# Performance work log

Measured on AMD Instinct MI355X. Metric: run time of the kernel, lower is better.

The kernel has to match this reference:

```python
import jax, jax.numpy as jnp
import numpy as np

PAD = 24
DR0, DR1 = 425.0, 905.0
DDIM = 128.0
N = 65536
H, W, D, FDIM = 176, 176, 132, 32
LAT, OUT, INP = 128, 257, 3
NUM_LAYERS = 8
SKIP = 4


def _linear_params(k, out_f, in_f):
    kw, kb = jax.random.split(k)
    s = 1.0 / np.sqrt(in_f)
    Wm = jax.random.uniform(kw, (out_f, in_f), jnp.float32, -s, s)
    bv = jax.random.uniform(kb, (out_f,), jnp.float32, -s, s)
    return Wm, bv


def setup_inputs() -> dict:
    key = jax.random.key(0)
    ks = jax.random.split(key, 20)
    world = jax.random.normal(ks[0], (N, 3), jnp.float32)
    u = jax.random.uniform(ks[1], (N,), jnp.float32, 2.0, 125.0)
    v = jax.random.uniform(ks[2], (N,), jnp.float32, 2.0, 125.0)
    d = jax.random.uniform(ks[3], (N,), jnp.float32, 440.0, 890.0)
    pixel = jnp.stack([u, v, d], axis=1)
    vol = jax.random.uniform(ks[4], (H, W, D, FDIM), jnp.float32)
    Wq, bq = _linear_params(ks[5], LAT, FDIM)
    inp = dict(sampled_points_world=world, sampled_points_pixel=pixel,
               feature_volume=vol, Wq=Wq, bq=bq)
    # MLP: layer0 3->128; layers 1..8: layer 4 is 128->125, else 128->128; layer9 128->257
    dims = [(LAT, INP)]
    for i in range(NUM_LAYERS):
        dims.append((LAT - INP if (i + 1) == SKIP else LAT, LAT))
    dims.append((OUT, LAT))
    for l, (o, i) in enumerate(dims):
        Wl, bl = _linear_params(ks[6 + l], o, i)
        inp[f"W{l}"] = Wl
        inp[f"b{l}"] = bl
    return inp


def softplus100(x):
    # torch Softplus(beta=100) with threshold=20: linear when 100*x > 20
    return jnp.where(x > 0.2, x, jnp.log1p(jnp.exp(jnp.minimum(x, 0.2) * 100.0)) / 100.0)


def query_layer(pixel, vol, Wq, bq):
    # q: padded/depth-normalized query coords [N,3]
    q = jnp.stack([pixel[:, 0] + PAD, pixel[:, 1] + PAD,
                   (pixel[:, 2] - DR0) / (DR1 - DR0) * DDIM], axis=1)
    base = jnp.floor(q).astype(jnp.int32)            # center = floor+0.5 for non-integer coords
    ax = jnp.arange(-1, 3)                           # window floor-1 .. floor+2 (4 per axis)
    offs = jnp.stack(jnp.meshgrid(ax, ax, ax, indexing='ij'), -1).reshape(-1, 3)  # [64,3]
    idx = base[:, None, :] + offs[None, :, :]        # [N,64,3]
    kcoord = idx.astype(q.dtype)
    vfeat = vol[idx[..., 0], idx[..., 1], idx[..., 2]]   # [N,64,F] gather
    sim = jnp.einsum('nkd,nd->nk', kcoord, q)            # key . query
    sim = sim / jnp.sum(sim, axis=1, keepdims=True)
    mixed = jnp.einsum('nk,nkf->nf', sim, vfeat)         # [N,F]
    feat = mixed / jnp.sum(mixed, axis=1, keepdims=True)
    return feat @ Wq.T + bq                              # [N,128]


def reference(sampled_points_world, sampled_points_pixel, feature_volume, Wq, bq,
              W0, b0, W1, b1, W2, b2, W3, b3, W4, b4,
              W5, b5, W6, b6, W7, b7, W8, b8, W9, b9):
    Ws = [W0, W1, W2, W3, W4, W5, W6, W7, W8, W9]
    bs = [b0, b1, b2, b3, b4, b5, b6, b7, b8, b9]
    bias = query_layer(sampled_points_pixel, feature_volume, Wq, bq)
    bias = bias / jnp.mean(jnp.abs(bias))
    x = sampled_points_world
    for l in range(NUM_LAYERS + 2):
        x = x @ Ws[l].T + bs[l]
        if l == SKIP:
            x = jnp.concatenate([x, sampled_points_world], axis=1)
        if l == 0:
            x = x * bias
        if l < NUM_LAYERS + 1:
            x = softplus100(x)
    return x
```

## Files before the change

kernel.cpp:

```cpp
#include <hip/hip_runtime.h>

#define NPTS 65536
#define VW 176
#define VD 132
#define FD 32

typedef _Float16 half8 __attribute__((ext_vector_type(8)));
typedef _Float16 h16x4 __attribute__((ext_vector_type(4)));
typedef float f32x4 __attribute__((ext_vector_type(4)));

#define OFF_WQ 0
#define OFF_L1 4096
#define OFF_L9 (4096 + 8 * 16384)
#define W16_TOTAL (4096 + 8 * 16384 + 32768)

struct Params {
    const float* W[10];
    const float* b[10];
};

__device__ __forceinline__ float sp100(float x) {
    if (x > 0.2f) return x;
    float e = __expf(x * 100.0f);
    return __logf(1.0f + e) * 0.01f;
}

__global__ __launch_bounds__(256) void prep_kernel(Params P, const float* __restrict__ Wq,
                                                   _Float16* __restrict__ w16) {
    const int i = blockIdx.x * 256 + threadIdx.x;
    if (i >= W16_TOTAL) return;
    if (i < 4096) { w16[i] = (_Float16)Wq[i]; return; }
    int j = i - 4096;
    if (j < 8 * 16384) {
        const int l = (j >> 14) + 1;
        const int r = (j & 16383) >> 7;
        float v = 0.0f;
        if (l != 4) v = P.W[l][j & 16383];
        else if (r < 125) v = P.W[4][j & 16383];
        w16[i] = (_Float16)v;
        return;
    }
    j -= 8 * 16384;
    w16[i] = (_Float16)P.W[9][j];
}

__global__ __launch_bounds__(256) void query_kernel(
    const float* __restrict__ pixel, const float* __restrict__ vol,
    _Float16* __restrict__ feat_out)
{
    const int tid = threadIdx.x;
    const int f = tid & 31;
    const int p = blockIdx.x * 8 + (tid >> 5);

    const float qx = pixel[p*3+0] + 24.0f;
    const float qy = pixel[p*3+1] + 24.0f;
    const float qz = (pixel[p*3+2] - 425.0f) / 480.0f * 128.0f;
    const int bx = (int)floorf(qx);
    const int by = (int)floorf(qy);
    const int bz = (int)floorf(qz);

    float mix0 = 0.0f, mix1 = 0.0f;
    #pragma unroll
    for (int dx = 0; dx < 4; ++dx) {
        const int i0 = bx + dx - 1;
        const float sx = (float)i0 * qx;
        #pragma unroll
        for (int dy = 0; dy < 4; ++dy) {
            const int i1 = by + dy - 1;
            const int rowbase = (i0 * VW + i1) * VD;
            const float sxy = sx + (float)i1 * qy;
            #pragma unroll
            for (int dz = 0; dz < 4; ++dz) {
                const int i2 = bz + dz - 1;
                const float sim = sxy + (float)i2 * qz;
                const float v = vol[(rowbase + i2) * FD + f];
                if (dx < 2) mix0 = fmaf(sim, v, mix0);
                else        mix1 = fmaf(sim, v, mix1);
            }
        }
    }
    const float mixed = mix0 + mix1;
    float tot = mixed;
    #pragma unroll
    for (int m = 16; m >= 1; m >>= 1) tot += __shfl_xor(tot, m, 32);
    feat_out[p*32 + f] = (_Float16)(mixed / tot);
}

__global__ __launch_bounds__(256) void bias_kernel(
    const _Float16* __restrict__ feat16, const _Float16* __restrict__ w16,
    const float* __restrict__ bq, float* __restrict__ sum_abs)
{
    const int tid  = threadIdx.x;
    const int lane = tid & 63;
    const int wid  = tid >> 6;
    const int n16  = lane & 15;
    const int kg   = lane >> 4;
    const int gm   = blockIdx.x * 64 + wid * 16;

    const half8 fa = *(const half8*)&feat16[(size_t)(gm + n16) * 32 + kg * 8];
    float s = 0.0f;
    #pragma unroll
    for (int ot = 0; ot < 8; ++ot) {
        const half8 wqf = *(const half8*)&w16[OFF_WQ + (ot*16 + n16) * 32 + kg * 8];
        f32x4 z = {};
        const f32x4 acc = __builtin_amdgcn_mfma_f32_16x16x32_f16(wqf, fa, z, 0, 0, 0);
        const int f0 = ot*16 + kg*4;
        const f32x4 bqv = *(const f32x4*)&bq[f0];
        #pragma unroll
        for (int r = 0; r < 4; ++r) s += fabsf(acc[r] + bqv[r]);
    }
    #pragma unroll
    for (int m = 32; m >= 1; m >>= 1) s += __shfl_xor(s, m, 64);
    __shared__ float part[4];
    if (lane == 0) part[wid] = s;
    __syncthreads();
    if (tid == 0) atomicAdd(sum_abs, part[0] + part[1] + part[2] + part[3]);
}

__global__ __launch_bounds__(256, 4) void mlp_kernel(
    const float* __restrict__ world, const _Float16* __restrict__ feat16,
    const _Float16* __restrict__ w16, const float* __restrict__ bq,
    const float* __restrict__ sum_abs, float* __restrict__ out, Params P)
{
    __shared__ __align__(16) _Float16 act[64 * 136];

    const int tid  = threadIdx.x;
    const int lane = tid & 63;
    const int wid  = tid >> 6;
    const int n16  = lane & 15;
    const int kg   = lane >> 4;
    const int wrow0 = wid * 16;
    const int gm    = blockIdx.x * 64 + wrow0;
    const float inv_mean = (float)NPTS * 128.0f / sum_abs[0];

    const float wx = world[(size_t)(gm + n16)*3 + 0];
    const float wy = world[(size_t)(gm + n16)*3 + 1];
    const float wz = world[(size_t)(gm + n16)*3 + 2];

    const int arow  = (wrow0 + n16) * 136;
    const int a_off = arow + kg * 8;

    {
        const half8 fa = *(const half8*)&feat16[(size_t)(gm + n16) * 32 + kg * 8];
        f32x4 acc[8];
        #pragma unroll
        for (int ot = 0; ot < 8; ++ot) {
            const half8 wqf = *(const half8*)&w16[OFF_WQ + (ot*16 + n16) * 32 + kg * 8];
            f32x4 z = {};
            acc[ot] = __builtin_amdgcn_mfma_f32_16x16x32_f16(wqf, fa, z, 0, 0, 0);
        }
        #pragma unroll
        for (int ot = 0; ot < 8; ++ot) {
            const int f0 = ot*16 + kg*4;
            const f32x4 b0v = *(const f32x4*)&P.b[0][f0];
            const f32x4 bqv = *(const f32x4*)&bq[f0];
            const f32x4 wA = *(const f32x4*)&P.W[0][f0*3 + 0];
            const f32x4 wB = *(const f32x4*)&P.W[0][f0*3 + 4];
            const f32x4 wC = *(const f32x4*)&P.W[0][f0*3 + 8];
            const float w0v[12] = {wA[0],wA[1],wA[2],wA[3],
                                   wB[0],wB[1],wB[2],wB[3],
                                   wC[0],wC[1],wC[2],wC[3]};
            h16x4 hv;
            #pragma unroll
            for (int r = 0; r < 4; ++r) {
                const float h = b0v[r] + w0v[3*r]*wx + w0v[3*r+1]*wy + w0v[3*r+2]*wz;
                const float bias = acc[ot][r] + bqv[r];
                hv[r] = (_Float16)sp100(h * bias * inv_mean);
            }
            *(h16x4*)&act[arow + f0] = hv;
        }
    }

    #pragma unroll 1
    for (int l = 1; l <= 8; ++l) {
        const _Float16* wl = &w16[OFF_L1 + (l - 1) * 16384];
        half8 a[4];
        #pragma unroll
        for (int c = 0; c < 4; ++c) a[c] = *(const half8*)&act[a_off + c*32];

        f32x4 acc[8] = {};
        #pragma unroll
        for (int c = 0; c < 4; ++c) {
            #pragma unroll
            for (int ot = 0; ot < 8; ++ot) {
                const half8 bf = *(const half8*)&wl[(ot*16 + n16)*128 + kg*8 + c*32];
                acc[ot] = __builtin_amdgcn_mfma_f32_16x16x32_f16(bf, a[c], acc[ot], 0, 0, 0);
            }
        }
        if (l != 4) {
            #pragma unroll
            for (int ot = 0; ot < 8; ++ot) {
                const int f0 = ot*16 + kg*4;
                const f32x4 bl4 = *(const f32x4*)&P.b[l][f0];
                h16x4 hv;
                #pragma unroll
                for (int r = 0; r < 4; ++r) hv[r] = (_Float16)sp100(acc[ot][r] + bl4[r]);
                *(h16x4*)&act[arow + f0] = hv;
            }
        } else {
            #pragma unroll
            for (int ot = 0; ot < 8; ++ot) {
                const int f0 = ot*16 + kg*4;
                h16x4 hv;
                #pragma unroll
                for (int r = 0; r < 4; ++r) {
                    const int f = f0 + r;
                    float v;
                    if (f < 125) v = acc[ot][r] + P.b[4][f];
                    else         v = (f == 125) ? wx : (f == 126) ? wy : wz;
                    hv[r] = (_Float16)sp100(v);
                }
                *(h16x4*)&act[arow + f0] = hv;
            }
        }
    }

    {
        half8 a[4];
        #pragma unroll
        for (int c = 0; c < 4; ++c) a[c] = *(const half8*)&act[a_off + c*32];

        #pragma unroll 1
        for (int hh = 0; hh < 2; ++hh) {
            f32x4 acc[8] = {};
            #pragma unroll
            for (int c = 0; c < 4; ++c) {
                #pragma unroll
                for (int ot = 0; ot < 8; ++ot) {
                    const half8 bf = *(const half8*)&w16[OFF_L9 + (hh*128 + ot*16 + n16)*128 + kg*8 + c*32];
                    acc[ot] = __builtin_amdgcn_mfma_f32_16x16x32_f16(a[c], bf, acc[ot], 0, 0, 0);
                }
            }
            #pragma unroll
            for (int ot = 0; ot < 8; ++ot) {
                const int col = ot*16 + n16;
                const float b9 = P.b[9][hh*128 + col];
                #pragma unroll
                for (int r = 0; r < 4; ++r) {
                    out[(size_t)(gm + kg*4 + r)*257 + hh*128 + col] = acc[ot][r] + b9;
                }
            }
        }
    }
    {
        const int rr = lane >> 2;
        const int q  = lane & 3;
        float s = 0.0f;
        #pragma unroll
        for (int j = 0; j < 32; ++j) {
            const int k = q*32 + j;
            s = fmaf((float)act[(wrow0 + rr)*136 + k], P.W[9][256*128 + k], s);
        }
        s += __shfl_xor(s, 1, 64);
        s += __shfl_xor(s, 2, 64);
        if (q == 0) out[(size_t)(gm + rr)*257 + 256] = P.b[9][256] + s;
    }
}

extern "C" void kernel_launch(void* const* d_in, const int* in_sizes, int n_in,
                              void* d_out, int out_size, void* d_ws, size_t ws_size,
                              hipStream_t stream) {
    const float* world = (const float*)d_in[0];
    const float* pixel = (const float*)d_in[1];
    const float* vol   = (const float*)d_in[2];
    const float* Wq    = (const float*)d_in[3];
    const float* bq    = (const float*)d_in[4];
    Params P;
    for (int l = 0; l < 10; ++l) {
        P.W[l] = (const float*)d_in[5 + 2*l];
        P.b[l] = (const float*)d_in[6 + 2*l];
    }
    float*    sum_abs = (float*)d_ws;
    _Float16* feat16  = (_Float16*)((char*)d_ws + 4096);
    _Float16* w16     = (_Float16*)((char*)d_ws + 4096 + (size_t)NPTS * 32 * 2);

    hipMemsetAsync(d_ws, 0, 256, stream);
    prep_kernel<<<(W16_TOTAL + 255) / 256, 256, 0, stream>>>(P, Wq, w16);
    query_kernel<<<NPTS / 8, 256, 0, stream>>>(pixel, vol, feat16);
    bias_kernel<<<NPTS / 64, 256, 0, stream>>>(feat16, w16, bq, sum_abs);
    mlp_kernel<<<NPTS / 64, 256, 0, stream>>>(world, feat16, w16, bq, sum_abs,
                                              (float*)d_out, P);
}
```

Before: 868.0 us.

## Vectorize volume gather to float4 per lane and fold weight prep into query kernel

The query kernel now has each thread handle four feature channels with 16-byte vector loads, so 8 lanes cover one point instead of 32, and the normalization shuffle shrinks to a width-8 reduction. Results are written as half4 stores. The separate fp16 weight-conversion kernel is removed and its work is done by the first 656 blocks of the query kernel, saving one launch. The trade-offs are more registers per thread and some load imbalance on the blocks that also do the conversion.

```diff
diff --git a/kernel.cpp b/kernel.cpp
--- a/kernel.cpp
+++ b/kernel.cpp
@@ -25,32 +25,33 @@
     return __logf(1.0f + e) * 0.01f;
 }
 
-__global__ __launch_bounds__(256) void prep_kernel(Params P, const float* __restrict__ Wq,
-                                                   _Float16* __restrict__ w16) {
-    const int i = blockIdx.x * 256 + threadIdx.x;
-    if (i >= W16_TOTAL) return;
-    if (i < 4096) { w16[i] = (_Float16)Wq[i]; return; }
-    int j = i - 4096;
-    if (j < 8 * 16384) {
-        const int l = (j >> 14) + 1;
-        const int r = (j & 16383) >> 7;
-        float v = 0.0f;
-        if (l != 4) v = P.W[l][j & 16383];
-        else if (r < 125) v = P.W[4][j & 16383];
-        w16[i] = (_Float16)v;
-        return;
-    }
-    j -= 8 * 16384;
-    w16[i] = (_Float16)P.W[9][j];
-}
-
 __global__ __launch_bounds__(256) void query_kernel(
     const float* __restrict__ pixel, const float* __restrict__ vol,
-    _Float16* __restrict__ feat_out)
+    _Float16* __restrict__ feat_out, Params P, const float* __restrict__ Wq,
+    _Float16* __restrict__ w16)
 {
+    if (blockIdx.x < 656) {
+        const int i = blockIdx.x * 256 + threadIdx.x;
+        if (i < 4096) { w16[i] = (_Float16)Wq[i]; }
+        else {
+            int j = i - 4096;
+            if (j < 8 * 16384) {
+                const int l = (j >> 14) + 1;
+                const int r = (j & 16383) >> 7;
+                float v = 0.0f;
+                if (l != 4) v = P.W[l][j & 16383];
+                else if (r < 125) v = P.W[4][j & 16383];
+                w16[i] = (_Float16)v;
+            } else {
+                j -= 8 * 16384;
+                w16[i] = (_Float16)P.W[9][j];
+            }
+        }
+    }
+
     const int tid = threadIdx.x;
-    const int f = tid & 31;
-    const int p = blockIdx.x * 8 + (tid >> 5);
+    const int f4  = tid & 7;
+    const int p   = blockIdx.x * 32 + (tid >> 3);
 
     const float qx = pixel[p*3+0] + 24.0f;
     const float qy = pixel[p*3+1] + 24.0f;
@@ -59,7 +60,7 @@
     const int by = (int)floorf(qy);
     const int bz = (int)floorf(qz);
 
-    float mix0 = 0.0f, mix1 = 0.0f;
+    f32x4 mix0 = {}, mix1 = {};
     #pragma unroll
     for (int dx = 0; dx < 4; ++dx) {
         const int i0 = bx + dx - 1;
@@ -73,17 +74,27 @@
             for (int dz = 0; dz < 4; ++dz) {
                 const int i2 = bz + dz - 1;
                 const float sim = sxy + (float)i2 * qz;
-                const float v = vol[(rowbase + i2) * FD + f];
-                if (dx < 2) mix0 = fmaf(sim, v, mix0);
-                else        mix1 = fmaf(sim, v, mix1);
-            }
-        }
-    }
-    const float mixed = mix0 + mix1;
-    float tot = mixed;
-    #pragma unroll
-    for (int m = 16; m >= 1; m >>= 1) tot += __shfl_xor(tot, m, 32);
-    feat_out[p*32 + f] = (_Float16)(mixed / tot);
+                const f32x4 v = *(const f32x4*)&vol[(rowbase + i2) * FD + f4 * 4];
+                if (dx < 2) { mix0[0] = fmaf(sim, v[0], mix0[0]);
+                              mix0[1] = fmaf(sim, v[1], mix0[1]);
+                              mix0[2] = fmaf(sim, v[2], mix0[2]);
+                              mix0[3] = fmaf(sim, v[3], mix0[3]); }
+                else        { mix1[0] = fmaf(sim, v[0], mix1[0]);
+                              mix1[1] = fmaf(sim, v[1], mix1[1]);
+                              mix1[2] = fmaf(sim, v[2], mix1[2]);
+                              mix1[3] = fmaf(sim, v[3], mix1[3]); }
+            }
+        }
+    }
+    const f32x4 mixed = mix0 + mix1;
+    float tot = (mixed[0] + mixed[1]) + (mixed[2] + mixed[3]);
+    #pragma unroll
+    for (int m = 4; m >= 1; m >>= 1) tot += __shfl_xor(tot, m, 8);
+    const float inv = 1.0f / tot;
+    h16x4 fo;
+    #pragma unroll
+    for (int r = 0; r < 4; ++r) fo[r] = (_Float16)(mixed[r] * inv);
+    *(h16x4*)&feat_out[p*32 + f4*4] = fo;
 }
 
 __global__ __launch_bounds__(256) void bias_kernel(
@@ -275,8 +286,7 @@
     _Float16* w16     = (_Float16*)((char*)d_ws + 4096 + (size_t)NPTS * 32 * 2);
 
     hipMemsetAsync(d_ws, 0, 256, stream);
-    prep_kernel<<<(W16_TOTAL + 255) / 256, 256, 0, stream>>>(P, Wq, w16);
-    query_kernel<<<NPTS / 8, 256, 0, stream>>>(pixel, vol, feat16);
+    query_kernel<<<NPTS / 32, 256, 0, stream>>>(pixel, vol, feat16, P, Wq, w16);
     bias_kernel<<<NPTS / 64, 256, 0, stream>>>(feat16, w16, bq, sum_abs);
     mlp_kernel<<<NPTS / 64, 256, 0, stream>>>(world, feat16, w16, bq, sum_abs,
                                               (float*)d_out, P);
```

New measurement: 873.1 us. No clear change (+0.6%).
